# Kernel tuning notes

Measured on AMD Instinct MI355X. Metric: run time of the kernel, lower is better.

Reference implementation:

```python
import jax, jax.numpy as jnp
import numpy as np

N, DIN, DOUT = 8192, 4096, 4096

def setup_inputs() -> dict:
    key = jax.random.key(0)
    k1, k2 = jax.random.split(key)
    x = jax.random.normal(k1, (N, DIN), dtype=jnp.float32)
    # ternary-ish weights; forward applies sign() via STE anyway
    weight = jax.random.normal(k2, (DOUT, DIN), dtype=jnp.float32)
    bias = jnp.zeros((DOUT,), dtype=jnp.float32)
    scale = jnp.ones((1,), dtype=jnp.float32)  # scale_init = 1.0
    return {"x": x, "weight": weight, "bias": bias, "scale": scale}


def reference(x, weight, bias, scale):
    # STE sign-quantization: value is sign(weight) in {-1,0,1},
    # gradient flows to weight as identity.
    w = weight - jax.lax.stop_gradient(weight - jnp.sign(weight))
    # fused ternary matmul + scale + bias: out = scale * (x @ w.T + bias)
    # (backward in the torch code scales grad for x, w, AND bias, implying
    #  bias sits inside the scale multiplier)
    return scale[0] * (jnp.matmul(x, w.T) + bias)
```

## Files before the change

### kernel.cpp

```cpp
#include <hip/hip_runtime.h>
#include <hip/hip_bf16.h>
#include <stdint.h>

#define M_DIM 8192
#define K_DIM 4096
#define N_DIM 4096

typedef int intx4 __attribute__((ext_vector_type(4)));

__global__ void cvt_fused_i8_kernel(const float* __restrict__ x,
                                    const float* __restrict__ w,
                                    signed char* __restrict__ xb,
                                    signed char* __restrict__ wb,
                                    float* __restrict__ row_scale) {
    const int b   = blockIdx.x;
    const int tid = threadIdx.x;
    if (b < M_DIM) {
        __shared__ float wmax[4];
        const float* xr = x + (size_t)b * K_DIM;
        float4 v[4];
#pragma unroll
        for (int i = 0; i < 4; ++i)
            v[i] = *(const float4*)(xr + tid * 4 + i * 1024);

        float am = 0.f;
#pragma unroll
        for (int i = 0; i < 4; ++i) {
            am = fmaxf(am, fabsf(v[i].x)); am = fmaxf(am, fabsf(v[i].y));
            am = fmaxf(am, fabsf(v[i].z)); am = fmaxf(am, fabsf(v[i].w));
        }
#pragma unroll
        for (int off = 32; off > 0; off >>= 1)
            am = fmaxf(am, __shfl_xor(am, off));
        if ((tid & 63) == 0) wmax[tid >> 6] = am;
        __syncthreads();
        am = fmaxf(fmaxf(wmax[0], wmax[1]), fmaxf(wmax[2], wmax[3]));
        am = fmaxf(am, 1e-30f);

        const float inv = 127.f / am;
#pragma unroll
        for (int i = 0; i < 4; ++i) {
            union { signed char c[4]; uint32_t u; } r;
            const float* vf = (const float*)&v[i];
#pragma unroll
            for (int k = 0; k < 4; ++k) {
                int q = (int)rintf(vf[k] * inv);
                q = q > 127 ? 127 : (q < -127 ? -127 : q);
                r.c[k] = (signed char)q;
            }
            *(uint32_t*)(xb + (size_t)b * K_DIM + tid * 4 + i * 1024) = r.u;
        }
        if (tid == 0) row_scale[b] = am * (1.f / 127.f);
    } else {
        size_t t = ((size_t)(b - M_DIM) * blockDim.x + tid) * 8;
        float4 a = *(const float4*)(w + t);
        float4 c = *(const float4*)(w + t + 4);
        union { signed char s[8]; uint2 u; } r;
        r.s[0] = (a.x > 0.f) - (a.x < 0.f); r.s[1] = (a.y > 0.f) - (a.y < 0.f);
        r.s[2] = (a.z > 0.f) - (a.z < 0.f); r.s[3] = (a.w > 0.f) - (a.w < 0.f);
        r.s[4] = (c.x > 0.f) - (c.x < 0.f); r.s[5] = (c.y > 0.f) - (c.y < 0.f);
        r.s[6] = (c.z > 0.f) - (c.z < 0.f); r.s[7] = (c.w > 0.f) - (c.w < 0.f);
        *(uint2*)(wb + t) = r.u;
    }
}

__device__ __forceinline__ void gld_lds16(const void* g, void* l) {
    __builtin_amdgcn_global_load_lds(
        (const __attribute__((address_space(1))) void*)g,
        (__attribute__((address_space(3))) void*)l,
        16, 0, 0);
}

__global__ void __launch_bounds__(512, 2)
gemm_i8_kernel(const signed char* __restrict__ A,
               const signed char* __restrict__ B,
               const float* __restrict__ bias,
               const float* __restrict__ scale,
               const float* __restrict__ row_scale,
               float* __restrict__ out) {
    __shared__ __attribute__((aligned(16))) signed char sA[4][256 * 64];
    __shared__ __attribute__((aligned(16))) signed char sB[4][256 * 64];

    const int tid  = threadIdx.x;
    const int lane = tid & 63;
    const int wave = tid >> 6;
    const int wm = wave >> 2;
    const int wn = wave & 3;
    const int g  = lane >> 4;
    const int mn = lane & 15;

    const int bid = blockIdx.x;
    const int swz = (bid & 7) * 64 + (bid >> 3);
    const int n_idx = swz & 15;
    const int m_idx = swz >> 4;
    const int rowBase = m_idx * 256;
    const int colBase = n_idx * 256;

    const int sc   = (lane & 3) ^ ((lane >> 3) & 3);
    const int srow = wave * 16 + (lane >> 2);
    const signed char* gA0 = A + (size_t)(rowBase + srow) * K_DIM + sc * 16;
    const signed char* gA1 = gA0 + (size_t)128 * K_DIM;
    const signed char* gB0 = B + (size_t)(colBase + srow) * K_DIM + sc * 16;
    const signed char* gB1 = gB0 + (size_t)128 * K_DIM;
    const int ldsR0 = wave * 1024;
    const int ldsR1 = 8192 + wave * 1024;

    const int fxor = (g ^ ((mn >> 1) & 3)) * 16;
    const int aoff = (wm * 128 + mn) * 64 + fxor;
    const int boff = (wn * 64 + mn) * 64 + fxor;

    intx4 acc0[4][4] = {};
    intx4 acc1[4][4] = {};

#pragma unroll
    for (int s = 0; s < 3; ++s) {
        const size_t kg = (size_t)s * 64;
        gld_lds16(gA0 + kg, &sA[s][ldsR0]);
        gld_lds16(gA1 + kg, &sA[s][ldsR1]);
        gld_lds16(gB0 + kg, &sB[s][ldsR0]);
        gld_lds16(gB1 + kg, &sB[s][ldsR1]);
    }
    asm volatile("s_waitcnt vmcnt(8)" ::: "memory");
    __builtin_amdgcn_s_barrier();

    for (int t = 0; t < 64; ++t) {
        const signed char* sAb = sA[t & 3];
        const signed char* sBb = sB[t & 3];
        signed char* pA = sA[(t + 3) & 3];
        signed char* pB = sB[(t + 3) & 3];
        const bool stage = t < 61;
        const size_t kg = (size_t)(t + 3) * 64;

        intx4 a0[4], b0[4];
#pragma unroll
        for (int i = 0; i < 4; ++i)
            a0[i] = *(const intx4*)(sAb + aoff + i * 1024);
#pragma unroll
        for (int j = 0; j < 4; ++j)
            b0[j] = *(const intx4*)(sBb + boff + j * 1024);
        if (stage) {
            gld_lds16(gA0 + kg, pA + ldsR0);
            gld_lds16(gA1 + kg, pA + ldsR1);
        }
        __builtin_amdgcn_s_barrier();
        asm volatile("s_waitcnt lgkmcnt(0)" ::: "memory");
        __builtin_amdgcn_sched_barrier(0);
        __builtin_amdgcn_s_setprio(1);
#pragma unroll
        for (int i = 0; i < 4; ++i)
#pragma unroll
            for (int j = 0; j < 4; ++j)
                acc0[i][j] = __builtin_amdgcn_mfma_i32_16x16x64_i8(
                    a0[i], b0[j], acc0[i][j], 0, 0, 0);
        __builtin_amdgcn_s_setprio(0);
        __builtin_amdgcn_sched_barrier(0);
        __builtin_amdgcn_s_barrier();

        intx4 a1[4];
#pragma unroll
        for (int i = 0; i < 4; ++i)
            a1[i] = *(const intx4*)(sAb + aoff + 4096 + i * 1024);
        if (stage) {
            gld_lds16(gB0 + kg, pB + ldsR0);
            gld_lds16(gB1 + kg, pB + ldsR1);
        }
        __builtin_amdgcn_s_barrier();
        asm volatile("s_waitcnt lgkmcnt(0)" ::: "memory");
        __builtin_amdgcn_sched_barrier(0);
        __builtin_amdgcn_s_setprio(1);
#pragma unroll
        for (int i = 0; i < 4; ++i)
#pragma unroll
            for (int j = 0; j < 4; ++j)
                acc1[i][j] = __builtin_amdgcn_mfma_i32_16x16x64_i8(
                    a1[i], b0[j], acc1[i][j], 0, 0, 0);
        __builtin_amdgcn_s_setprio(0);
        __builtin_amdgcn_sched_barrier(0);

        if (t < 61)       asm volatile("s_waitcnt vmcnt(8)" ::: "memory");
        else if (t == 61) asm volatile("s_waitcnt vmcnt(4)" ::: "memory");
        else if (t == 62) asm volatile("s_waitcnt vmcnt(0)" ::: "memory");
        __builtin_amdgcn_s_barrier();
    }

    const float s = scale[0];
#pragma unroll
    for (int j = 0; j < 4; ++j) {
        const int gcol = colBase + wn * 64 + j * 16 + mn;
        const float bv = bias[gcol];
#pragma unroll
        for (int i = 0; i < 4; ++i) {
            {
                const int grow0 = rowBase + wm * 128 + i * 16 + g * 4;
                const float4 rs4 = *(const float4*)(row_scale + grow0);
                const float rs[4] = {rs4.x, rs4.y, rs4.z, rs4.w};
#pragma unroll
                for (int r = 0; r < 4; ++r)
                    __builtin_nontemporal_store(
                        s * ((float)acc0[i][j][r] * rs[r] + bv),
                        out + (size_t)(grow0 + r) * N_DIM + gcol);
            }
            {
                const int grow1 = rowBase + wm * 128 + 64 + i * 16 + g * 4;
                const float4 rs4 = *(const float4*)(row_scale + grow1);
                const float rs[4] = {rs4.x, rs4.y, rs4.z, rs4.w};
#pragma unroll
                for (int r = 0; r < 4; ++r)
                    __builtin_nontemporal_store(
                        s * ((float)acc1[i][j][r] * rs[r] + bv),
                        out + (size_t)(grow1 + r) * N_DIM + gcol);
            }
        }
    }
}

__global__ void fallback_kernel(const float* __restrict__ x,
                                const float* __restrict__ w,
                                const float* __restrict__ bias,
                                const float* __restrict__ scale,
                                float* __restrict__ out) {
    int col = blockIdx.x * 64 + (threadIdx.x & 63);
    int row = blockIdx.y * 4 + (threadIdx.x >> 6);
    const float* xr = x + (size_t)row * K_DIM;
    const float* wr = w + (size_t)col * K_DIM;
    float acc = 0.f;
    for (int k = 0; k < K_DIM; k += 4) {
        float4 a = *(const float4*)(xr + k);
        float4 b = *(const float4*)(wr + k);
        acc += a.x * (b.x > 0.f ? 1.f : (b.x < 0.f ? -1.f : 0.f));
        acc += a.y * (b.y > 0.f ? 1.f : (b.y < 0.f ? -1.f : 0.f));
        acc += a.z * (b.z > 0.f ? 1.f : (b.z < 0.f ? -1.f : 0.f));
        acc += a.w * (b.w > 0.f ? 1.f : (b.w < 0.f ? -1.f : 0.f));
    }
    out[(size_t)row * N_DIM + col] = scale[0] * (acc + bias[col]);
}

extern "C" void kernel_launch(void* const* d_in, const int* in_sizes, int n_in,
                              void* d_out, int out_size, void* d_ws, size_t ws_size,
                              hipStream_t stream) {
    const float* x     = (const float*)d_in[0];
    const float* w     = (const float*)d_in[1];
    const float* bias  = (const float*)d_in[2];
    const float* scale = (const float*)d_in[3];
    float* out = (float*)d_out;

    const size_t xb_bytes = (size_t)M_DIM * K_DIM;
    const size_t wb_bytes = (size_t)N_DIM * K_DIM;
    const size_t need = xb_bytes + wb_bytes + M_DIM * sizeof(float);

    if (ws_size >= need) {
        signed char* xb = (signed char*)d_ws;
        signed char* wb = xb + xb_bytes;
        float* row_scale = (float*)(wb + wb_bytes);
        const unsigned w_blocks = (unsigned)((size_t)N_DIM * K_DIM / 8 / 256);
        cvt_fused_i8_kernel<<<dim3(M_DIM + w_blocks), 256, 0, stream>>>(
            x, w, xb, wb, row_scale);
        gemm_i8_kernel<<<dim3((M_DIM / 256) * (N_DIM / 256)), 512, 0, stream>>>(
            xb, wb, bias, scale, row_scale, out);
    } else {
        dim3 grid(N_DIM / 64, M_DIM / 4);
        fallback_kernel<<<grid, 256, 0, stream>>>(x, w, bias, scale, out);
    }
}
```

Measured before the change: 419.7 us.

## Switch int8 GEMM to 32x32x32 MFMA with register double-buffered LDS fragments

Replaces the 16x16x64 int8 MFMA tiles with 32x32x32 tiles (intx16 accumulators), which lowers the number of LDS fragment reads per MFMA FLOP. The main loop is restructured so fragments for the next k-slice are prefetched into registers while the current MFMAs run, and the two intra-iteration barriers with lgkmcnt waits are removed. Global-to-LDS staging is merged into one issue point with adjusted vmcnt thresholds. This risks higher register pressure, possible LDS read hazards from fewer barriers, and a different epilogue store pattern.

```diff
diff --git a/kernel.cpp b/kernel.cpp
--- a/kernel.cpp
+++ b/kernel.cpp
@@ -6,7 +6,8 @@
 #define K_DIM 4096
 #define N_DIM 4096
 
-typedef int intx4 __attribute__((ext_vector_type(4)));
+typedef int intx4  __attribute__((ext_vector_type(4)));
+typedef int intx16 __attribute__((ext_vector_type(16)));
 
 __global__ void cvt_fused_i8_kernel(const float* __restrict__ x,
                                     const float* __restrict__ w,
@@ -86,15 +87,13 @@
     const int wave = tid >> 6;
     const int wm = wave >> 2;
     const int wn = wave & 3;
-    const int g  = lane >> 4;
-    const int mn = lane & 15;
+    const int r5 = lane & 31;
+    const int hi = lane >> 5;
 
     const int bid = blockIdx.x;
     const int swz = (bid & 7) * 64 + (bid >> 3);
-    const int n_idx = swz & 15;
-    const int m_idx = swz >> 4;
-    const int rowBase = m_idx * 256;
-    const int colBase = n_idx * 256;
+    const int rowBase = (swz >> 4) * 256;
+    const int colBase = (swz & 15) * 256;
 
     const int sc   = (lane & 3) ^ ((lane >> 3) & 3);
     const int srow = wave * 16 + (lane >> 2);
@@ -105,12 +104,15 @@
     const int ldsR0 = wave * 1024;
     const int ldsR1 = 8192 + wave * 1024;
 
-    const int fxor = (g ^ ((mn >> 1) & 3)) * 16;
-    const int aoff = (wm * 128 + mn) * 64 + fxor;
-    const int boff = (wn * 64 + mn) * 64 + fxor;
-
-    intx4 acc0[4][4] = {};
-    intx4 acc1[4][4] = {};
+    const int fsw = (r5 >> 1) & 3;
+    const int ckE = ((hi + 0) ^ fsw) * 16;
+    const int ckO = ((hi + 2) ^ fsw) * 16;
+    const int aOff = (wm * 128 + r5) * 64;
+    const int bOff = (wn * 64 + r5) * 64;
+
+    intx16 acc[4][2] = {};
+    intx4 fa[4], fb[2];
+    intx4 oa[4], ob[2];
 
 #pragma unroll
     for (int s = 0; s < 3; ++s) {
@@ -120,95 +122,89 @@
         gld_lds16(gB0 + kg, &sB[s][ldsR0]);
         gld_lds16(gB1 + kg, &sB[s][ldsR1]);
     }
-    asm volatile("s_waitcnt vmcnt(8)" ::: "memory");
+    asm volatile("s_waitcnt vmcnt(4)" ::: "memory");
     __builtin_amdgcn_s_barrier();
+
+#pragma unroll
+    for (int mt = 0; mt < 4; ++mt)
+        fa[mt] = *(const intx4*)(&sA[0][0] + aOff + mt * 2048 + ckE);
+#pragma unroll
+    for (int nt = 0; nt < 2; ++nt)
+        fb[nt] = *(const intx4*)(&sB[0][0] + bOff + nt * 2048 + ckE);
 
     for (int t = 0; t < 64; ++t) {
         const signed char* sAb = sA[t & 3];
         const signed char* sBb = sB[t & 3];
-        signed char* pA = sA[(t + 3) & 3];
-        signed char* pB = sB[(t + 3) & 3];
-        const bool stage = t < 61;
-        const size_t kg = (size_t)(t + 3) * 64;
-
-        intx4 a0[4], b0[4];
-#pragma unroll
-        for (int i = 0; i < 4; ++i)
-            a0[i] = *(const intx4*)(sAb + aoff + i * 1024);
-#pragma unroll
-        for (int j = 0; j < 4; ++j)
-            b0[j] = *(const intx4*)(sBb + boff + j * 1024);
-        if (stage) {
+        const signed char* sAn = sA[(t + 1) & 3];
+        const signed char* sBn = sB[(t + 1) & 3];
+
+#pragma unroll
+        for (int mt = 0; mt < 4; ++mt)
+            oa[mt] = *(const intx4*)(sAb + aOff + mt * 2048 + ckO);
+#pragma unroll
+        for (int nt = 0; nt < 2; ++nt)
+            ob[nt] = *(const intx4*)(sBb + bOff + nt * 2048 + ckO);
+        if (t < 61) {
+            signed char* pA = sA[(t + 3) & 3];
+            signed char* pB = sB[(t + 3) & 3];
+            const size_t kg = (size_t)(t + 3) * 64;
             gld_lds16(gA0 + kg, pA + ldsR0);
             gld_lds16(gA1 + kg, pA + ldsR1);
-        }
-        __builtin_amdgcn_s_barrier();
-        asm volatile("s_waitcnt lgkmcnt(0)" ::: "memory");
-        __builtin_amdgcn_sched_barrier(0);
-        __builtin_amdgcn_s_setprio(1);
-#pragma unroll
-        for (int i = 0; i < 4; ++i)
-#pragma unroll
-            for (int j = 0; j < 4; ++j)
-                acc0[i][j] = __builtin_amdgcn_mfma_i32_16x16x64_i8(
-                    a0[i], b0[j], acc0[i][j], 0, 0, 0);
-        __builtin_amdgcn_s_setprio(0);
-        __builtin_amdgcn_sched_barrier(0);
-        __builtin_amdgcn_s_barrier();
-
-        intx4 a1[4];
-#pragma unroll
-        for (int i = 0; i < 4; ++i)
-            a1[i] = *(const intx4*)(sAb + aoff + 4096 + i * 1024);
-        if (stage) {
             gld_lds16(gB0 + kg, pB + ldsR0);
             gld_lds16(gB1 + kg, pB + ldsR1);
         }
+        __builtin_amdgcn_sched_barrier(0);
+
+        __builtin_amdgcn_s_setprio(1);
+#pragma unroll
+        for (int mt = 0; mt < 4; ++mt)
+#pragma unroll
+            for (int nt = 0; nt < 2; ++nt)
+                acc[mt][nt] = __builtin_amdgcn_mfma_i32_32x32x32_i8(
+                    fa[mt], fb[nt], acc[mt][nt], 0, 0, 0);
+        __builtin_amdgcn_s_setprio(0);
+        __builtin_amdgcn_sched_barrier(0);
+
+#pragma unroll
+        for (int mt = 0; mt < 4; ++mt)
+            fa[mt] = *(const intx4*)(sAn + aOff + mt * 2048 + ckE);
+#pragma unroll
+        for (int nt = 0; nt < 2; ++nt)
+            fb[nt] = *(const intx4*)(sBn + bOff + nt * 2048 + ckE);
+        __builtin_amdgcn_sched_barrier(0);
+
+        __builtin_amdgcn_s_setprio(1);
+#pragma unroll
+        for (int mt = 0; mt < 4; ++mt)
+#pragma unroll
+            for (int nt = 0; nt < 2; ++nt)
+                acc[mt][nt] = __builtin_amdgcn_mfma_i32_32x32x32_i8(
+                    oa[mt], ob[nt], acc[mt][nt], 0, 0, 0);
+        __builtin_amdgcn_s_setprio(0);
+        __builtin_amdgcn_sched_barrier(0);
+
+        if (t < 61)       asm volatile("s_waitcnt vmcnt(4)" ::: "memory");
+        else if (t == 61) asm volatile("s_waitcnt vmcnt(0)" ::: "memory");
         __builtin_amdgcn_s_barrier();
-        asm volatile("s_waitcnt lgkmcnt(0)" ::: "memory");
-        __builtin_amdgcn_sched_barrier(0);
-        __builtin_amdgcn_s_setprio(1);
-#pragma unroll
-        for (int i = 0; i < 4; ++i)
-#pragma unroll
-            for (int j = 0; j < 4; ++j)
-                acc1[i][j] = __builtin_amdgcn_mfma_i32_16x16x64_i8(
-                    a1[i], b0[j], acc1[i][j], 0, 0, 0);
-        __builtin_amdgcn_s_setprio(0);
-        __builtin_amdgcn_sched_barrier(0);
-
-        if (t < 61)       asm volatile("s_waitcnt vmcnt(8)" ::: "memory");
-        else if (t == 61) asm volatile("s_waitcnt vmcnt(4)" ::: "memory");
-        else if (t == 62) asm volatile("s_waitcnt vmcnt(0)" ::: "memory");
-        __builtin_amdgcn_s_barrier();
     }
 
     const float s = scale[0];
 #pragma unroll
-    for (int j = 0; j < 4; ++j) {
-        const int gcol = colBase + wn * 64 + j * 16 + mn;
+    for (int nt = 0; nt < 2; ++nt) {
+        const int gcol = colBase + wn * 64 + nt * 32 + r5;
         const float bv = bias[gcol];
 #pragma unroll
-        for (int i = 0; i < 4; ++i) {
-            {
-                const int grow0 = rowBase + wm * 128 + i * 16 + g * 4;
-                const float4 rs4 = *(const float4*)(row_scale + grow0);
+        for (int mt = 0; mt < 4; ++mt) {
+#pragma unroll
+            for (int q = 0; q < 4; ++q) {
+                const int row0 = rowBase + wm * 128 + mt * 32 + q * 8 + hi * 4;
+                const float4 rs4 = *(const float4*)(row_scale + row0);
                 const float rs[4] = {rs4.x, rs4.y, rs4.z, rs4.w};
 #pragma unroll
                 for (int r = 0; r < 4; ++r)
                     __builtin_nontemporal_store(
-                        s * ((float)acc0[i][j][r] * rs[r] + bv),
-                        out + (size_t)(grow0 + r) * N_DIM + gcol);
-            }
-            {
-                const int grow1 = rowBase + wm * 128 + 64 + i * 16 + g * 4;
-                const float4 rs4 = *(const float4*)(row_scale + grow1);
-                const float rs[4] = {rs4.x, rs4.y, rs4.z, rs4.w};
-#pragma unroll
-                for (int r = 0; r < 4; ++r)
-                    __builtin_nontemporal_store(
-                        s * ((float)acc1[i][j][r] * rs[r] + bv),
-                        out + (size_t)(grow1 + r) * N_DIM + gcol);
+                        s * ((float)acc[mt][nt][q * 4 + r] * rs[r] + bv),
+                        out + (size_t)(row0 + r) * N_DIM + gcol);
             }
         }
     }
```

New measurement: 405.1 us. -3.5%, faster.
